# Kernel optimization log

Measured on AMD Instinct MI355X. Metric: run time of the kernel, lower is better.

## Reference

```python
import jax, jax.numpy as jnp
import numpy as np

K = 5  # kNN neighbors (includes self, as in PyG knn(x, x, k))


def _lin_bn(x, W, b, s, h):
    # Linear -> ReLU -> BatchNorm (inference, folded to scale s / shift h)
    return jax.nn.relu(x @ W + b) * s + h


def _knn_idx(x, k):
    # x: [B, N, F] -> idx: [B, N, k] indices of k nearest points (incl. self)
    x2 = jnp.sum(x * x, axis=-1)  # [B, N]
    d = x2[:, :, None] + x2[:, None, :] - 2.0 * jnp.einsum('bnf,bmf->bnm', x, x)
    return jax.lax.top_k(-d, k)[1]


def _edge_conv(x, k, edge_mlp):
    # DynamicEdgeConv: knn graph, message mlp([x_i, x_j - x_i]), max-aggregate
    idx = _knn_idx(x, k)                                   # [B, N, k]
    xj = jax.vmap(lambda xb, ib: xb[ib])(x, idx)           # [B, N, k, F]
    xi = jnp.broadcast_to(x[:, :, None, :], xj.shape)
    e = jnp.concatenate([xi, xj - xi], axis=-1)            # [B, N, k, 2F]
    return jnp.max(edge_mlp(e), axis=2)                    # [B, N, F_out]


def _forward(pos, w1a, b1a, s1a, h1a, w1b, b1b, s1b, h1b, w1c, b1c, s1c, h1c,
             w2, b2, s2, h2, wl, bl, sl, hl,
             wm1, bm1, sm1, hm1, wm2, bm2, sm2, hm2, wout, bout):
    mlp1 = lambda e: _lin_bn(_lin_bn(_lin_bn(e, w1a, b1a, s1a, h1a),
                                     w1b, b1b, s1b, h1b), w1c, b1c, s1c, h1c)
    mlp2 = lambda e: _lin_bn(e, w2, b2, s2, h2)
    x1 = _edge_conv(pos, K, mlp1)                          # [B, N, 64]
    x2 = _edge_conv(x1, K, mlp2)                           # [B, N, 128]
    out = _lin_bn(jnp.concatenate([x1, x2], axis=-1), wl, bl, sl, hl)  # [B,N,1024]
    out = jnp.max(out, axis=1)                             # global max pool -> [B,1024]
    out = _lin_bn(out, wm1, bm1, sm1, hm1)                 # Dropout = identity (eval)
    out = _lin_bn(out, wm2, bm2, sm2, hm2)
    return out @ wout + bout                               # [B, n_classes]


def setup_inputs() -> dict:
    key = jax.random.key(0)
    ks = jax.random.split(key, 32)
    B, N = 32, 2048
    rn = lambda k, sh: jax.random.normal(k, sh, dtype=jnp.float32)
    ru = lambda k, sh: jax.random.uniform(k, sh, dtype=jnp.float32)
    d = {'pos': rn(ks[0], (B, N, 3))}
    i = 1
    for nm, cin, cout in [('1a', 6, 64), ('1b', 64, 64), ('1c', 64, 64),
                          ('2', 128, 128), ('l', 192, 1024),
                          ('m1', 1024, 512), ('m2', 512, 256)]:
        d['w' + nm] = rn(ks[i], (cin, cout)) / np.sqrt(cin); i += 1
        d['b' + nm] = rn(ks[i], (cout,)) * 0.1; i += 1
        d['s' + nm] = ru(ks[i], (cout,)) + 0.5; i += 1
        d['h' + nm] = rn(ks[i], (cout,)) * 0.1; i += 1
    d['wout'] = rn(ks[i], (256, 2)) / np.sqrt(256.0); i += 1
    d['bout'] = rn(ks[i], (2,)) * 0.1
    return d


def reference(pos, w1a, b1a, s1a, h1a, w1b, b1b, s1b, h1b, w1c, b1c, s1c, h1c,
              w2, b2, s2, h2, wl, bl, sl, hl,
              wm1, bm1, sm1, hm1, wm2, bm2, sm2, hm2, wout, bout):
    return _forward(pos, w1a, b1a, s1a, h1a, w1b, b1b, s1b, h1b, w1c, b1c, s1c, h1c,
                    w2, b2, s2, h2, wl, bl, sl, hl,
                    wm1, bm1, sm1, hm1, wm2, bm2, sm2, hm2, wout, bout)
```

## Files before the change

kernel.cpp:

```cpp
#include <hip/hip_runtime.h>

#define DEV __device__ __forceinline__
DEV float relu_(float x) { return fmaxf(x, 0.0f); }

typedef __attribute__((ext_vector_type(4))) float f32x4;
typedef __attribute__((ext_vector_type(8))) __bf16 bf16x8;

DEV unsigned short bfbits(__bf16 b) { union { unsigned short s; __bf16 b; } x; x.b = b; return x.s; }
DEV __bf16 bffrom(unsigned short s) { union { unsigned short s; __bf16 b; } x; x.s = s; return x.b; }

DEV void knn_insert(float (&bd)[5], int (&bi)[5], float d, int j) {
  if (d >= bd[4]) return;
  bd[4] = d; bi[4] = j;
#pragma unroll
  for (int p = 4; p > 0; --p) {
    if (bd[p] < bd[p - 1]) {
      float td = bd[p]; bd[p] = bd[p - 1]; bd[p - 1] = td;
      int ti = bi[p]; bi[p] = bi[p - 1]; bi[p - 1] = ti;
    }
  }
}

DEV void knn_insert_bl(float (&bd)[5], int (&bi)[5], float d, int j) {
#pragma unroll
  for (int p = 0; p < 5; ++p) {
    bool lt = d < bd[p];
    float nd = lt ? d : bd[p];
    float cd = lt ? bd[p] : d;
    int ni = lt ? j : bi[p];
    int ci = lt ? bi[p] : j;
    bd[p] = nd; d = cd;
    bi[p] = ni; j = ci;
  }
}

DEV void ins5(float (&b)[5], float x) {
  b[4] = __builtin_amdgcn_fmed3f(b[3], b[4], x);
  b[3] = __builtin_amdgcn_fmed3f(b[2], b[3], x);
  b[2] = __builtin_amdgcn_fmed3f(b[1], b[2], x);
  b[1] = __builtin_amdgcn_fmed3f(b[0], b[1], x);
  b[0] = fminf(b[0], x);
}

__global__ __launch_bounds__(256) void k_front(
    const float* __restrict__ pos, const float* __restrict__ w1a,
    const float* __restrict__ b1a, const float* __restrict__ w1b,
    const float* __restrict__ w1c, const float* __restrict__ w2,
    const float* __restrict__ wl,
    int* __restrict__ idx1, float* __restrict__ uR, float* __restrict__ vR,
    __bf16* __restrict__ wfh, __bf16* __restrict__ wfl,
    __bf16* __restrict__ wph, __bf16* __restrict__ wpl,
    __bf16* __restrict__ wlb) {
  __shared__ __align__(16) float smem[9472];
  int tid = threadIdx.x;
  int blk = blockIdx.x;
  if (blk < 2048) {
    float* ps = smem;
    float* sqs = smem + 6144;
    float* md = smem + 8192;
    int* mi = (int*)(smem + 8832);
    int b = blk >> 6, qc = blk & 63;
    const float* src = pos + b * 6144;
    for (int u = tid; u < 6144; u += 256) ps[u] = src[u];
    __syncthreads();
    for (int u = tid; u < 2048; u += 256) {
      float x = ps[u * 3], y = ps[u * 3 + 1], z = ps[u * 3 + 2];
      sqs[u] = fmaf(z, z, fmaf(y, y, x * x));
    }
    __syncthreads();
    int q = tid & 31, sub = tid >> 5;
    int qi = qc * 32 + q;
    float qx = ps[qi * 3], qy = ps[qi * 3 + 1], qz = ps[qi * 3 + 2];
    float qsq = sqs[qi];
    float bp[5] = {1e30f, 1e30f, 1e30f, 1e30f, 1e30f};
    int j0 = sub * 256;
    for (int j = j0; j < j0 + 256; ++j) {
      float px = ps[j * 3], py = ps[j * 3 + 1], pz = ps[j * 3 + 2];
      float dot = fmaf(qz, pz, fmaf(qy, py, qx * px));
      float d = fmaxf((qsq + sqs[j]) - 2.0f * dot, 0.0f);
      unsigned u = (__float_as_uint(d) & 0xFFFFFF00u) | (unsigned)(j & 255);
      ins5(bp, __uint_as_float(u));
    }
    float bd[5]; int bi[5];
#pragma unroll
    for (int k = 0; k < 5; ++k) {
      unsigned u = __float_as_uint(bp[k]);
      bd[k] = __uint_as_float(u & 0xFFFFFF00u);
      bi[k] = j0 + (int)(u & 255u);
    }
    for (int half = 4; half >= 1; half >>= 1) {
      __syncthreads();
      if (sub >= half && sub < 2 * half) {
        int slot = (q * 4 + (sub - half)) * 5;
#pragma unroll
        for (int k = 0; k < 5; ++k) { md[slot + k] = bd[k]; mi[slot + k] = bi[k]; }
      }
      __syncthreads();
      if (sub < half) {
        int slot = (q * 4 + sub) * 5;
#pragma unroll
        for (int k = 0; k < 5; ++k) knn_insert_bl(bd, bi, md[slot + k], mi[slot + k]);
      }
    }
    if (sub == 0) {
      int* op = idx1 + (b * 2048 + qi) * 5;
#pragma unroll
      for (int k = 0; k < 5; ++k) op[k] = bi[k];
    }
  } else if (blk < 3072) {
    float* wAs = smem;
    float* bs = smem + 384;
    float* uS = smem + 448;
    float* vS = smem + 4800;
    for (int u = tid; u < 384; u += 256) wAs[u] = w1a[u];
    if (tid < 64) bs[tid] = b1a[tid];
    __syncthreads();
    int lane = tid & 63, fq = tid >> 6;
    int p0 = (blk - 2048) * 64;
    int p = p0 + lane;
    float x0 = pos[p * 3], x1 = pos[p * 3 + 1], x2 = pos[p * 3 + 2];
#pragma unroll
    for (int m = 0; m < 16; ++m) {
      int f = fq * 16 + m;
      float wt0 = wAs[f], wt1 = wAs[64 + f], wt2 = wAs[128 + f];
      float wb0 = wAs[192 + f], wb1 = wAs[256 + f], wb2 = wAs[320 + f];
      float uval = bs[f];
      uval = fmaf(x0, wt0 - wb0, uval);
      uval = fmaf(x1, wt1 - wb1, uval);
      uval = fmaf(x2, wt2 - wb2, uval);
      uS[lane * 68 + f] = uval;
      vS[lane * 68 + f] = fmaf(x2, wb2, fmaf(x1, wb1, x0 * wb0));
    }
    __syncthreads();
#pragma unroll
    for (int it = 0; it < 4; ++it) {
      int g = it * 1024 + tid * 4;
      int pl = g >> 6, f = g & 63;
      float4 uu = *(const float4*)(uS + pl * 68 + f);
      float4 vv = *(const float4*)(vS + pl * 68 + f);
      *(float4*)(uR + (size_t)p0 * 64 + g) = uu;
      *(float4*)(vR + (size_t)p0 * 64 + g) = vv;
    }
  } else {
    int pblk = blk - 3072;
    if (pblk < 4) {
      int t = pblk * 256 + tid;
      int m = t >> 9;
      int rem = t & 511;
      int nb = rem >> 7;
      int rem2 = rem & 127;
      int s = rem2 >> 6, lane = rem2 & 63;
      int k0 = s * 32 + (lane >> 4) * 8;
      int c = nb * 16 + (lane & 15);
      const float* W = m ? w1c : w1b;
      __bf16 oh[8], ol[8];
#pragma unroll
      for (int j = 0; j < 8; ++j) {
        float val = W[(k0 + j) * 64 + c];
        __bf16 h = (__bf16)val;
        oh[j] = h;
        ol[j] = (__bf16)(val - (float)h);
      }
      size_t off = (size_t)m * 4096 + ((size_t)((nb * 2 + s) * 64 + lane)) * 8;
      *(uint4*)(wfh + off) = *(const uint4*)oh;
      *(uint4*)(wfl + off) = *(const uint4*)ol;
    } else if (pblk < 12) {
      int t = (pblk - 4) * 256 + tid;
      int nb = t >> 7;
      int rem = t & 127;
      int ks = rem >> 6, lane = rem & 63;
      int k0 = ks * 32 + (lane >> 4) * 8;
      int col16 = lane & 15;
      __bf16 oh[8], ol[8];
#pragma unroll
      for (int j = 0; j < 8; ++j) {
        int k = k0 + j;
        float val;
        if (nb < 8) {
          int c = nb * 16 + col16;
          val = w2[k * 128 + c] - w2[(64 + k) * 128 + c];
        } else {
          int c = (nb - 8) * 16 + col16;
          val = w2[(64 + k) * 128 + c];
        }
        __bf16 h = (__bf16)val;
        oh[j] = h;
        ol[j] = (__bf16)(val - (float)h);
      }
      *(uint4*)(wph + (size_t)t * 8) = *(const uint4*)oh;
      *(uint4*)(wpl + (size_t)t * 8) = *(const uint4*)ol;
    } else {
      int t = (pblk - 12) * 256 + tid;
      int nt = t / 3072;
      int rem = t - nt * 3072;
      int ks = rem / 512;
      int rem2 = rem - ks * 512;
      int nb = rem2 >> 6, lane = rem2 & 63;
      int k0 = ks * 32 + (lane >> 4) * 8;
      int n = nt * 128 + nb * 16 + (lane & 15);
      __bf16 o[8];
#pragma unroll
      for (int j = 0; j < 8; ++j) o[j] = (__bf16)wl[(k0 + j) * 1024 + n];
      *(uint4*)(wlb + (size_t)t * 8) = *(const uint4*)o;
    }
  }
}

__global__ __launch_bounds__(256) void k_edge1(
    const int* __restrict__ idx1, const float* __restrict__ uR,
    const float* __restrict__ vR,
    const float* __restrict__ s1a, const float* __restrict__ h1a,
    const float* __restrict__ b1b, const float* __restrict__ s1b,
    const float* __restrict__ h1b,
    const float* __restrict__ b1c, const float* __restrict__ s1c,
    const float* __restrict__ h1c,
    const __bf16* __restrict__ wfh, const __bf16* __restrict__ wfl,
    __bf16* __restrict__ xh, __bf16* __restrict__ xl,
    float* __restrict__ sqo, __bf16* __restrict__ xb) {
  __shared__ __align__(16) __bf16 Wh[8192], Wl[8192];
  __shared__ __align__(16) unsigned h2b[4 * 1088];
  int tid = threadIdx.x;
  int w = tid >> 6, lane = tid & 63;
  int quad = lane >> 4, lm = lane & 15;
#pragma unroll
  for (int it = 0; it < 4; ++it) {
    int u4 = it * 256 + tid;
    *(uint4*)(Wh + (size_t)u4 * 8) = *(const uint4*)(wfh + (size_t)u4 * 8);
    *(uint4*)(Wl + (size_t)u4 * 8) = *(const uint4*)(wfl + (size_t)u4 * 8);
  }
  int p0 = blockIdx.x * 64;
  int b = p0 >> 11;
  size_t bb = (size_t)b * 2048;
  int edge = p0 + w * 16 + lm;
  float sA[2][8], hA[2][8];
#pragma unroll
  for (int s = 0; s < 2; ++s)
#pragma unroll
    for (int j = 0; j < 8; ++j) {
      int k = s * 32 + quad * 8 + j;
      sA[s][j] = s1a[k]; hA[s][j] = h1a[k];
    }
  float bB[4], sB[4], hB[4], bC[4], sC[4], hC[4];
#pragma unroll
  for (int nb = 0; nb < 4; ++nb) {
    int c = nb * 16 + lm;
    bB[nb] = b1b[c]; sB[nb] = s1b[c]; hB[nb] = h1b[c];
    bC[nb] = b1c[c]; sC[nb] = s1c[c]; hC[nb] = h1c[c];
  }
  unsigned* h2w = h2b + w * 1088;
  f32x4 mmax[4];
#pragma unroll
  for (int nb = 0; nb < 4; ++nb)
    mmax[nb] = (f32x4){-3.4e38f, -3.4e38f, -3.4e38f, -3.4e38f};
  __syncthreads();
  const float* urow = uR + (size_t)edge * 64;
  for (int kk = 0; kk < 5; ++kk) {
    int jn = idx1[edge * 5 + kk];
    const float* vrow = vR + (bb + jn) * 64;
    bf16x8 Ah[2], Al[2];
#pragma unroll
    for (int s = 0; s < 2; ++s) {
      int off = s * 32 + quad * 8;
      float4 u0 = *(const float4*)(urow + off);
      float4 u1 = *(const float4*)(urow + off + 4);
      float4 v0 = *(const float4*)(vrow + off);
      float4 v1 = *(const float4*)(vrow + off + 4);
      float uv[8] = {u0.x + v0.x, u0.y + v0.y, u0.z + v0.z, u0.w + v0.w,
                     u1.x + v1.x, u1.y + v1.y, u1.z + v1.z, u1.w + v1.w};
      __bf16 th[8], tl[8];
#pragma unroll
      for (int j = 0; j < 8; ++j) {
        float val = relu_(uv[j]) * sA[s][j] + hA[s][j];
        __bf16 hb = (__bf16)val;
        th[j] = hb;
        tl[j] = (__bf16)(val - (float)hb);
      }
      Ah[s] = *(const bf16x8*)th;
      Al[s] = *(const bf16x8*)tl;
    }
#pragma unroll
    for (int nb = 0; nb < 4; ++nb) {
      bf16x8 Bh0 = *(const bf16x8*)(Wh + ((size_t)((nb * 2 + 0) * 64 + lane)) * 8);
      bf16x8 Bh1 = *(const bf16x8*)(Wh + ((size_t)((nb * 2 + 1) * 64 + lane)) * 8);
      bf16x8 Bl0 = *(const bf16x8*)(Wl + ((size_t)((nb * 2 + 0) * 64 + lane)) * 8);
      bf16x8 Bl1 = *(const bf16x8*)(Wl + ((size_t)((nb * 2 + 1) * 64 + lane)) * 8);
      f32x4 a2 = {0.f, 0.f, 0.f, 0.f};
      a2 = __builtin_amdgcn_mfma_f32_16x16x32_bf16(Ah[0], Bh0, a2, 0, 0, 0);
      a2 = __builtin_amdgcn_mfma_f32_16x16x32_bf16(Ah[1], Bh1, a2, 0, 0, 0);
      a2 = __builtin_amdgcn_mfma_f32_16x16x32_bf16(Ah[0], Bl0, a2, 0, 0, 0);
      a2 = __builtin_amdgcn_mfma_f32_16x16x32_bf16(Ah[1], Bl1, a2, 0, 0, 0);
      a2 = __builtin_amdgcn_mfma_f32_16x16x32_bf16(Al[0], Bh0, a2, 0, 0, 0);
      a2 = __builtin_amdgcn_mfma_f32_16x16x32_bf16(Al[1], Bh1, a2, 0, 0, 0);
#pragma unroll
      for (int r = 0; r < 4; ++r) {
        float vv2 = relu_(a2[r] + bB[nb]) * sB[nb] + hB[nb];
        __bf16 hb = (__bf16)vv2;
        __bf16 lb = (__bf16)(vv2 - (float)hb);
        h2w[(quad * 4 + r) * 68 + nb * 16 + lm] =
            (unsigned)bfbits(hb) | ((unsigned)bfbits(lb) << 16);
      }
    }
    bf16x8 A3h[2], A3l[2];
#pragma unroll
    for (int s = 0; s < 2; ++s) {
      const unsigned* rp = h2w + lm * 68 + s * 32 + quad * 8;
      uint4 da = *(const uint4*)rp;
      uint4 db = *(const uint4*)(rp + 4);
      unsigned dw[8] = {da.x, da.y, da.z, da.w, db.x, db.y, db.z, db.w};
      __bf16 th[8], tl[8];
#pragma unroll
      for (int j = 0; j < 8; ++j) {
        th[j] = bffrom((unsigned short)(dw[j] & 0xFFFFu));
        tl[j] = bffrom((unsigned short)(dw[j] >> 16));
      }
      A3h[s] = *(const bf16x8*)th;
      A3l[s] = *(const bf16x8*)tl;
    }
#pragma unroll
    for (int nb = 0; nb < 4; ++nb) {
      bf16x8 Bh0 = *(const bf16x8*)(Wh + 4096 + ((size_t)((nb * 2 + 0) * 64 + lane)) * 8);
      bf16x8 Bh1 = *(const bf16x8*)(Wh + 4096 + ((size_t)((nb * 2 + 1) * 64 + lane)) * 8);
      bf16x8 Bl0 = *(const bf16x8*)(Wl + 4096 + ((size_t)((nb * 2 + 0) * 64 + lane)) * 8);
      bf16x8 Bl1 = *(const bf16x8*)(Wl + 4096 + ((size_t)((nb * 2 + 1) * 64 + lane)) * 8);
      f32x4 a3 = {0.f, 0.f, 0.f, 0.f};
      a3 = __builtin_amdgcn_mfma_f32_16x16x32_bf16(A3h[0], Bh0, a3, 0, 0, 0);
      a3 = __builtin_amdgcn_mfma_f32_16x16x32_bf16(A3h[1], Bh1, a3, 0, 0, 0);
      a3 = __builtin_amdgcn_mfma_f32_16x16x32_bf16(A3h[0], Bl0, a3, 0, 0, 0);
      a3 = __builtin_amdgcn_mfma_f32_16x16x32_bf16(A3h[1], Bl1, a3, 0, 0, 0);
      a3 = __builtin_amdgcn_mfma_f32_16x16x32_bf16(A3l[0], Bh0, a3, 0, 0, 0);
      a3 = __builtin_amdgcn_mfma_f32_16x16x32_bf16(A3l[1], Bh1, a3, 0, 0, 0);
#pragma unroll
      for (int r = 0; r < 4; ++r) mmax[nb][r] = fmaxf(mmax[nb][r], a3[r]);
    }
  }
  float sqp[4] = {0.f, 0.f, 0.f, 0.f};
#pragma unroll
  for (int nb = 0; nb < 4; ++nb) {
    int c = nb * 16 + lm;
#pragma unroll
    for (int r = 0; r < 4; ++r) {
      float vv3 = relu_(mmax[nb][r] + bC[nb]) * sC[nb] + hC[nb];
      sqp[r] = fmaf(vv3, vv3, sqp[r]);
      __bf16 hb = (__bf16)vv3;
      __bf16 lb = (__bf16)(vv3 - (float)hb);
      int n = p0 + w * 16 + quad * 4 + r;
      xh[(size_t)n * 64 + c] = hb;
      xl[(size_t)n * 64 + c] = lb;
      xb[(size_t)n * 192 + c] = hb;
    }
  }
#pragma unroll
  for (int r = 0; r < 4; ++r) {
    float s = sqp[r];
    s += __shfl_xor(s, 1);
    s += __shfl_xor(s, 2);
    s += __shfl_xor(s, 4);
    s += __shfl_xor(s, 8);
    if (lm == 0) sqo[p0 + w * 16 + quad * 4 + r] = s;
  }
}

__global__ __launch_bounds__(256) void k_mid(const __bf16* __restrict__ xh,
                                             const __bf16* __restrict__ xl,
                                             const float* __restrict__ sq,
                                             __bf16* __restrict__ scratch,
                                             const __bf16* __restrict__ wph,
                                             const __bf16* __restrict__ wpl,
                                             __bf16* __restrict__ Pb,
                                             __bf16* __restrict__ Qb) {
  __shared__ __align__(16) float smem[6656];
  int tid = threadIdx.x;
  int w = tid >> 6, lane = tid & 63;
  int quad = lane >> 4, lm = lane & 15;
  if (blockIdx.x < 2048) {
    __bf16* Bh = (__bf16*)smem;
    __bf16* Bl = (__bf16*)(smem + 2304);
    float* sqs = smem + 4608;
    int blk = blockIdx.x;
    int b = blk >> 6;
    int w6 = blk & 63;
    int qc = w6 >> 1, g = w6 & 1;
    int q0 = qc * 64;
    size_t bb = (size_t)b * 2048;
    for (int u = tid; u < 512; u += 256)
      *(float4*)(sqs + u * 4) = *(const float4*)(sq + bb + u * 4);
    const __bf16* qh = xh + (bb + q0 + w * 16 + lm) * 64 + quad * 8;
    const __bf16* ql = xl + (bb + q0 + w * 16 + lm) * 64 + quad * 8;
    bf16x8 Ah0 = *(const bf16x8*)(qh);
    bf16x8 Ah1 = *(const bf16x8*)(qh + 32);
    bf16x8 Al0 = *(const bf16x8*)(ql);
    bf16x8 Al1 = *(const bf16x8*)(ql + 32);
    __syncthreads();
    float qsq[4];
#pragma unroll
    for (int r = 0; r < 4; ++r) qsq[r] = sqs[q0 + w * 16 + quad * 4 + r];
    float bp[4][5];
#pragma unroll
    for (int r = 0; r < 4; ++r)
#pragma unroll
      for (int k = 0; k < 5; ++k) bp[r][k] = 1e30f;
    for (int it = 0; it < 16; ++it) {
      int ct = g * 16 + it;
#pragma unroll
      for (int pass = 0; pass < 2; ++pass) {
        int unit = pass * 256 + tid;
        int n = unit >> 3, cc = unit & 7;
        const __bf16* gsrc = xh + (bb + ct * 64 + n) * 64 + cc * 8;
        const __bf16* gsrl = xl + (bb + ct * 64 + n) * 64 + cc * 8;
        *(uint4*)(Bh + n * 72 + cc * 8) = *(const uint4*)gsrc;
        *(uint4*)(Bl + n * 72 + cc * 8) = *(const uint4*)gsrl;
      }
      __syncthreads();
#pragma unroll
      for (int nt = 0; nt < 4; ++nt) {
        const __bf16* bph = Bh + (nt * 16 + lm) * 72 + quad * 8;
        const __bf16* bpl = Bl + (nt * 16 + lm) * 72 + quad * 8;
        bf16x8 Bh0 = *(const bf16x8*)(bph);
        bf16x8 Bh1 = *(const bf16x8*)(bph + 32);
        bf16x8 Bl0 = *(const bf16x8*)(bpl);
        bf16x8 Bl1 = *(const bf16x8*)(bpl + 32);
        f32x4 acc = {0.f, 0.f, 0.f, 0.f};
        acc = __builtin_amdgcn_mfma_f32_16x16x32_bf16(Ah0, Bh0, acc, 0, 0, 0);
        acc = __builtin_amdgcn_mfma_f32_16x16x32_bf16(Ah1, Bh1, acc, 0, 0, 0);
        acc = __builtin_amdgcn_mfma_f32_16x16x32_bf16(Ah0, Bl0, acc, 0, 0, 0);
        acc = __builtin_amdgcn_mfma_f32_16x16x32_bf16(Ah1, Bl1, acc, 0, 0, 0);
        acc = __builtin_amdgcn_mfma_f32_16x16x32_bf16(Al0, Bh0, acc, 0, 0, 0);
        acc = __builtin_amdgcn_mfma_f32_16x16x32_bf16(Al1, Bh1, acc, 0, 0, 0);
        float csq = sqs[ct * 64 + nt * 16 + lm];
        unsigned key = (unsigned)(it * 4 + nt);
#pragma unroll
        for (int r = 0; r < 4; ++r) {
          float d = fmaxf((qsq[r] + csq) - 2.0f * acc[r], 0.0f);
          unsigned u = (__float_as_uint(d) & 0xFFFFFFC0u) | key;
          ins5(bp[r], __uint_as_float(u));
        }
      }
      __syncthreads();
    }
    float bd[4][5];
    int bi[4][5];
#pragma unroll
    for (int r = 0; r < 4; ++r)
#pragma unroll
      for (int k = 0; k < 5; ++k) {
        unsigned u = __float_as_uint(bp[r][k]);
        bd[r][k] = __uint_as_float(u & 0xFFFFFFC0u);
        bi[r][k] = (g << 10) + (((int)(u & 63u)) << 4) + lm;
      }
    for (int m = 1; m <= 8; m <<= 1) {
#pragma unroll
      for (int r = 0; r < 4; ++r) {
        float od[5]; int oi[5];
#pragma unroll
        for (int k = 0; k < 5; ++k) {
          od[k] = __shfl_xor(bd[r][k], m);
          oi[k] = __shfl_xor(bi[r][k], m);
        }
#pragma unroll
        for (int k = 0; k < 5; ++k) knn_insert(bd[r], bi[r], od[k], oi[k]);
      }
    }
    if (lm == 0) {
#pragma unroll
      for (int r = 0; r < 4; ++r) {
        int qi = q0 + w * 16 + quad * 4 + r;
        uint2* sp = (uint2*)((char*)scratch + (size_t)(bb + qi) * 384 + 128 + g * 40);
#pragma unroll
        for (int k = 0; k < 5; ++k) {
          uint2 v;
          v.x = __float_as_uint(bd[r][k]);
          v.y = (unsigned)bi[r][k];
          sp[k] = v;
        }
      }
    }
  } else {
    __bf16* Wh = (__bf16*)smem;
    __bf16* Wl = (__bf16*)(smem + 2048);
    int n0 = (blockIdx.x - 2048) * 64;
    const __bf16* ah = xh + (size_t)(n0 + w * 16 + lm) * 64 + quad * 8;
    const __bf16* al = xl + (size_t)(n0 + w * 16 + lm) * 64 + quad * 8;
    bf16x8 Ah0 = *(const bf16x8*)(ah);
    bf16x8 Ah1 = *(const bf16x8*)(ah + 32);
    bf16x8 Al0 = *(const bf16x8*)(al);
    bf16x8 Al1 = *(const bf16x8*)(al + 32);
    for (int chunk = 0; chunk < 4; ++chunk) {
      __syncthreads();
#pragma unroll
      for (int it = 0; it < 2; ++it) {
        int unit = it * 256 + tid;
        *(uint4*)(Wh + (size_t)unit * 8) =
            *(const uint4*)(wph + (size_t)chunk * 4096 + (size_t)unit * 8);
        *(uint4*)(Wl + (size_t)unit * 8) =
            *(const uint4*)(wpl + (size_t)chunk * 4096 + (size_t)unit * 8);
      }
      __syncthreads();
#pragma unroll
      for (int nb4 = 0; nb4 < 4; ++nb4) {
        int nb = chunk * 4 + nb4;
        bf16x8 Bh0 = *(const bf16x8*)(Wh + ((size_t)(nb4 * 2 + 0) * 64 + lane) * 8);
        bf16x8 Bh1 = *(const bf16x8*)(Wh + ((size_t)(nb4 * 2 + 1) * 64 + lane) * 8);
        bf16x8 Bl0 = *(const bf16x8*)(Wl + ((size_t)(nb4 * 2 + 0) * 64 + lane) * 8);
        bf16x8 Bl1 = *(const bf16x8*)(Wl + ((size_t)(nb4 * 2 + 1) * 64 + lane) * 8);
        f32x4 acc = {0.f, 0.f, 0.f, 0.f};
        acc = __builtin_amdgcn_mfma_f32_16x16x32_bf16(Ah0, Bh0, acc, 0, 0, 0);
        acc = __builtin_amdgcn_mfma_f32_16x16x32_bf16(Ah1, Bh1, acc, 0, 0, 0);
        acc = __builtin_amdgcn_mfma_f32_16x16x32_bf16(Ah0, Bl0, acc, 0, 0, 0);
        acc = __builtin_amdgcn_mfma_f32_16x16x32_bf16(Ah1, Bl1, acc, 0, 0, 0);
        acc = __builtin_amdgcn_mfma_f32_16x16x32_bf16(Al0, Bh0, acc, 0, 0, 0);
        acc = __builtin_amdgcn_mfma_f32_16x16x32_bf16(Al1, Bh1, acc, 0, 0, 0);
        bool isP = (nb < 8);
        __bf16* base = isP ? Pb : Qb;
        int col = (isP ? nb : nb - 8) * 16 + lm;
#pragma unroll
        for (int r = 0; r < 4; ++r) {
          int n = n0 + w * 16 + quad * 4 + r;
          base[(size_t)n * 128 + col] = (__bf16)acc[r];
        }
      }
    }
  }
}

__global__ __launch_bounds__(256) void k_kmerge(const __bf16* __restrict__ scratch,
                                                int* __restrict__ idx2) {
  int n = blockIdx.x * 256 + threadIdx.x;
  const uint2* sp = (const uint2*)((const char*)scratch + (size_t)n * 384 + 128);
  float bd[5]; int bi[5];
#pragma unroll
  for (int k = 0; k < 5; ++k) {
    uint2 v = sp[k];
    bd[k] = __uint_as_float(v.x);
    bi[k] = (int)v.y;
  }
#pragma unroll
  for (int k = 0; k < 5; ++k) {
    uint2 v = sp[5 + k];
    knn_insert(bd, bi, __uint_as_float(v.x), (int)v.y);
  }
  int* op = idx2 + (size_t)n * 5;
#pragma unroll
  for (int k = 0; k < 5; ++k) op[k] = bi[k];
}

__global__ __launch_bounds__(256) void k_gmax(const __bf16* __restrict__ Pb,
                                              const __bf16* __restrict__ Qb,
                                              const int* __restrict__ idx2,
                                              const float* __restrict__ b2,
                                              const float* __restrict__ s2,
                                              const float* __restrict__ h2v,
                                              __bf16* __restrict__ xb) {
  int tid = threadIdx.x;
  int c4 = tid & 31, p = tid >> 5;
  int n = blockIdx.x * 8 + p;
  int b = n >> 11;
  const int* ip = idx2 + n * 5;
  int c0 = c4 * 4;
  float m[4] = {-3.4e38f, -3.4e38f, -3.4e38f, -3.4e38f};
#pragma unroll
  for (int k = 0; k < 5; ++k) {
    int j = ip[k];
    uint2 q = *(const uint2*)(Qb + ((size_t)(b * 2048 + j)) * 128 + c0);
    m[0] = fmaxf(m[0], (float)bffrom((unsigned short)(q.x & 0xFFFFu)));
    m[1] = fmaxf(m[1], (float)bffrom((unsigned short)(q.x >> 16)));
    m[2] = fmaxf(m[2], (float)bffrom((unsigned short)(q.y & 0xFFFFu)));
    m[3] = fmaxf(m[3], (float)bffrom((unsigned short)(q.y >> 16)));
  }
  uint2 pv = *(const uint2*)(Pb + (size_t)n * 128 + c0);
  float pvf[4] = {(float)bffrom((unsigned short)(pv.x & 0xFFFFu)),
                  (float)bffrom((unsigned short)(pv.x >> 16)),
                  (float)bffrom((unsigned short)(pv.y & 0xFFFFu)),
                  (float)bffrom((unsigned short)(pv.y >> 16))};
  __bf16 o[4];
#pragma unroll
  for (int i = 0; i < 4; ++i) {
    float v = pvf[i] + m[i] + b2[c0 + i];
    o[i] = (__bf16)(relu_(v) * s2[c0 + i] + h2v[c0 + i]);
  }
  uint2 ov;
  ov.x = (unsigned)bfbits(o[0]) | ((unsigned)bfbits(o[1]) << 16);
  ov.y = (unsigned)bfbits(o[2]) | ((unsigned)bfbits(o[3]) << 16);
  *(uint2*)(xb + (size_t)n * 192 + 64 + c0) = ov;
}

__global__ __launch_bounds__(256) void k_linl_mfma(const __bf16* __restrict__ xb,
                                                   const __bf16* __restrict__ wlb,
                                                   float* __restrict__ pool_part) {
  __shared__ __align__(16) __bf16 Aall[12288];
  __shared__ __align__(16) __bf16 Bl[8192];
  int tid = threadIdx.x;
  int w = tid >> 6, lane = tid & 63;
  int mg = blockIdx.x;
  int n0 = mg << 6;
  int quad = lane >> 4, lm = lane & 15;
#pragma unroll
  for (int it = 0; it < 6; ++it) {
    int unit = it * 256 + tid;
    int mb = unit / 384;
    int rem = unit - mb * 384;
    int ks = rem >> 6, ln = rem & 63;
    int lmm = ln & 15, qd = ln >> 4;
    const uint4* ga = (const uint4*)(xb + (size_t)(n0 + mb * 16 + lmm) * 192 + ks * 32 + qd * 8);
    *(uint4*)(Aall + ((size_t)(mb * 6 + ks) * 64 + ln) * 8) = *ga;
  }
  for (int ng = 0; ng < 4; ++ng) {
    f32x4 acc[4][4];
#pragma unroll
    for (int i = 0; i < 4; ++i)
#pragma unroll
      for (int j = 0; j < 4; ++j) acc[i][j] = (f32x4){0.f, 0.f, 0.f, 0.f};
    for (int ks = 0; ks < 6; ++ks) {
      __syncthreads();
#pragma unroll
      for (int nt2 = 0; nt2 < 2; ++nt2) {
#pragma unroll
        for (int u = 0; u < 2; ++u) {
          int unit = u * 256 + tid;
          const uint4* gb = (const uint4*)(wlb + ((size_t)((ng * 2 + nt2) * 6 + ks)) * 4096 + (size_t)unit * 8);
          *(uint4*)(Bl + (size_t)nt2 * 4096 + (size_t)unit * 8) = *gb;
        }
      }
      __syncthreads();
      bf16x8 af[4], bfr[4];
#pragma unroll
      for (int i = 0; i < 4; ++i)
        af[i] = *(const bf16x8*)(Aall + ((size_t)(i * 6 + ks) * 64 + lane) * 8);
      int nt2 = w >> 1, nbb = (w & 1) * 4;
#pragma unroll
      for (int j = 0; j < 4; ++j)
        bfr[j] = *(const bf16x8*)(Bl + (size_t)nt2 * 4096 + ((size_t)((nbb + j) * 64 + lane)) * 8);
#pragma unroll
      for (int i = 0; i < 4; ++i)
#pragma unroll
        for (int j = 0; j < 4; ++j)
          acc[i][j] = __builtin_amdgcn_mfma_f32_16x16x32_bf16(af[i], bfr[j], acc[i][j], 0, 0, 0);
    }
#pragma unroll
    for (int j = 0; j < 4; ++j) {
      float m = -3.4e38f;
#pragma unroll
      for (int i = 0; i < 4; ++i)
#pragma unroll
        for (int r = 0; r < 4; ++r) m = fmaxf(m, acc[i][j][r]);
      m = fmaxf(m, __shfl_xor(m, 16));
      m = fmaxf(m, __shfl_xor(m, 32));
      if (quad == 0) {
        int ch = ng * 256 + (w >> 1) * 128 + (w & 1) * 64 + j * 16 + lm;
        pool_part[(size_t)mg * 1024 + ch] = m;
      }
    }
  }
}

__global__ __launch_bounds__(256) void k_pool(const float* __restrict__ pool_part,
                                              const float* __restrict__ bl,
                                              const float* __restrict__ sl,
                                              const float* __restrict__ hl,
                                              float* __restrict__ p,
                                              float* __restrict__ out) {
  int b = blockIdx.x >> 2, cb = blockIdx.x & 3;
  int c = cb * 256 + threadIdx.x;
  const float* src = pool_part + (size_t)(b * 32) * 1024 + c;
  float m0 = -3.4e38f, m1 = -3.4e38f, m2 = -3.4e38f, m3 = -3.4e38f;
#pragma unroll
  for (int t = 0; t < 32; t += 4) {
    m0 = fmaxf(m0, src[(size_t)t * 1024]);
    m1 = fmaxf(m1, src[(size_t)(t + 1) * 1024]);
    m2 = fmaxf(m2, src[(size_t)(t + 2) * 1024]);
    m3 = fmaxf(m3, src[(size_t)(t + 3) * 1024]);
  }
  float m = fmaxf(fmaxf(m0, m1), fmaxf(m2, m3));
  p[b * 1024 + c] = relu_(m + bl[c]) * sl[c] + hl[c];
  if (blockIdx.x == 0 && threadIdx.x < 64) out[threadIdx.x] = 0.0f;
}

__global__ __launch_bounds__(256) void k_m1(const float* __restrict__ p,
                                            const float* __restrict__ wm1,
                                            const float* __restrict__ bm1,
                                            const float* __restrict__ sm1,
                                            const float* __restrict__ hm1,
                                            float* __restrict__ h1) {
  __shared__ float p_s[1024];
  __shared__ float red[4][64];
  int b = blockIdx.x >> 3, cb = blockIdx.x & 7;
  int tid = threadIdx.x;
  for (int u = tid; u < 1024; u += 256) p_s[u] = p[b * 1024 + u];
  __syncthreads();
  int c64 = tid & 63, q = tid >> 6;
  int C = cb * 64 + c64;
  int f0 = q * 256;
  const float* W = wm1 + (size_t)f0 * 512 + C;
  float a[8] = {0.f, 0.f, 0.f, 0.f, 0.f, 0.f, 0.f, 0.f};
  for (int f = 0; f < 256; f += 8) {
#pragma unroll
    for (int u = 0; u < 8; ++u)
      a[u] = fmaf(p_s[f0 + f + u], W[(size_t)(f + u) * 512], a[u]);
  }
  red[q][c64] = ((a[0] + a[1]) + (a[2] + a[3])) + ((a[4] + a[5]) + (a[6] + a[7]));
  __syncthreads();
  if (tid < 64) {
    float t = (red[0][tid] + red[1][tid]) + (red[2][tid] + red[3][tid]);
    int C2 = cb * 64 + tid;
    h1[b * 512 + C2] = relu_(t + bm1[C2]) * sm1[C2] + hm1[C2];
  }
}

__global__ __launch_bounds__(256) void k_m2o(const float* __restrict__ h1,
                                             const float* __restrict__ wm2,
                                             const float* __restrict__ bm2,
                                             const float* __restrict__ sm2,
                                             const float* __restrict__ hm2,
                                             const float* __restrict__ wout,
                                             const float* __restrict__ bout,
                                             float* __restrict__ out) {
  __shared__ float h1_s[512];
  __shared__ float red[4][64];
  int b = blockIdx.x >> 2, cb = blockIdx.x & 3;
  int tid = threadIdx.x;
  for (int u = tid; u < 512; u += 256) h1_s[u] = h1[b * 512 + u];
  __syncthreads();
  int c64 = tid & 63, q = tid >> 6;
  int C = cb * 64 + c64;
  int f0 = q * 128;
  const float* W = wm2 + (size_t)f0 * 256 + C;
  float a[4] = {0.f, 0.f, 0.f, 0.f};
  for (int f = 0; f < 128; f += 4) {
#pragma unroll
    for (int u = 0; u < 4; ++u)
      a[u] = fmaf(h1_s[f0 + f + u], W[(size_t)(f + u) * 256], a[u]);
  }
  red[q][c64] = (a[0] + a[1]) + (a[2] + a[3]);
  __syncthreads();
  if (tid < 64) {
    float t = (red[0][tid] + red[1][tid]) + (red[2][tid] + red[3][tid]);
    int C2 = cb * 64 + tid;
    float h2v = relu_(t + bm2[C2]) * sm2[C2] + hm2[C2];
    float2 wv = *(const float2*)(wout + C2 * 2);
    float v0 = h2v * wv.x, v1 = h2v * wv.y;
#pragma unroll
    for (int m = 1; m < 64; m <<= 1) {
      v0 += __shfl_xor(v0, m);
      v1 += __shfl_xor(v1, m);
    }
    if (tid == 0) {
      if (cb == 0) { v0 += bout[0]; v1 += bout[1]; }
      atomicAdd(&out[b * 2], v0);
      atomicAdd(&out[b * 2 + 1], v1);
    }
  }
}

extern "C" void kernel_launch(void* const* d_in, const int* in_sizes, int n_in,
                              void* d_out, int out_size, void* d_ws, size_t ws_size,
                              hipStream_t stream) {
  const float* pos = (const float*)d_in[0];
  const float* w1a = (const float*)d_in[1];
  const float* b1a = (const float*)d_in[2];
  const float* s1a = (const float*)d_in[3];
  const float* h1a = (const float*)d_in[4];
  const float* w1b = (const float*)d_in[5];
  const float* b1b = (const float*)d_in[6];
  const float* s1b = (const float*)d_in[7];
  const float* h1b = (const float*)d_in[8];
  const float* w1c = (const float*)d_in[9];
  const float* b1c = (const float*)d_in[10];
  const float* s1c = (const float*)d_in[11];
  const float* h1c = (const float*)d_in[12];
  const float* w2 = (const float*)d_in[13];
  const float* b2 = (const float*)d_in[14];
  const float* s2 = (const float*)d_in[15];
  const float* h2 = (const float*)d_in[16];
  const float* wl = (const float*)d_in[17];
  const float* bl = (const float*)d_in[18];
  const float* sl = (const float*)d_in[19];
  const float* hl = (const float*)d_in[20];
  const float* wm1 = (const float*)d_in[21];
  const float* bm1 = (const float*)d_in[22];
  const float* sm1 = (const float*)d_in[23];
  const float* hm1 = (const float*)d_in[24];
  const float* wm2 = (const float*)d_in[25];
  const float* bm2 = (const float*)d_in[26];
  const float* sm2 = (const float*)d_in[27];
  const float* hm2 = (const float*)d_in[28];
  const float* wout = (const float*)d_in[29];
  const float* bout = (const float*)d_in[30];
  float* out = (float*)d_out;

  float* base = (float*)d_ws;
  __bf16* xh = (__bf16*)base;
  __bf16* xl = (__bf16*)(base + 2097152);
  float* PbF = base + 4194304;
  float* QbF = PbF + 4194304;
  float* xbF = QbF + 4194304;
  int* idx = (int*)(xbF + 6291456);
  float* sq = (float*)(idx + 327680);
  __bf16* wph = (__bf16*)(sq + 65536);
  __bf16* wpl = (__bf16*)(sq + 65536 + 8192);
  __bf16* wfh = (__bf16*)(sq + 65536 + 16384);
  __bf16* wfl = (__bf16*)(sq + 65536 + 20480);
  __bf16* wlb = (__bf16*)(sq + 65536 + 24576);
  __bf16* Pb = (__bf16*)PbF;
  __bf16* Qb = (__bf16*)QbF;
  __bf16* xb = (__bf16*)xbF;
  float* uR = PbF;
  float* vR = QbF;
  float* pool_part = base + 131072;
  float* p_pool = base + 1179648;
  float* h1g = base + 1212416;

  k_front<<<3180, 256, 0, stream>>>(pos, w1a, b1a, w1b, w1c, w2, wl, idx, uR, vR,
                                    wfh, wfl, wph, wpl, wlb);
  k_edge1<<<1024, 256, 0, stream>>>(idx, uR, vR, s1a, h1a, b1b, s1b, h1b, b1c,
                                    s1c, h1c, wfh, wfl, xh, xl, sq, xb);
  k_mid<<<3072, 256, 0, stream>>>(xh, xl, sq, xb, wph, wpl, Pb, Qb);
  k_kmerge<<<256, 256, 0, stream>>>(xb, idx);
  k_gmax<<<8192, 256, 0, stream>>>(Pb, Qb, idx, b2, s2, h2, xb);
  k_linl_mfma<<<1024, 256, 0, stream>>>(xb, wlb, pool_part);
  k_pool<<<128, 256, 0, stream>>>(pool_part, bl, sl, hl, p_pool, out);
  k_m1<<<256, 256, 0, stream>>>(p_pool, wm1, bm1, sm1, hm1, h1g);
  k_m2o<<<128, 256, 0, stream>>>(h1g, wm2, bm2, sm2, hm2, wout, bout, out);
}
```

Before: 363.2 us.

## Transpose point cloud to SoA, prefetch kNN tiles, merge top-5 with sorting network

```diff
diff --git a/kernel.cpp b/kernel.cpp
--- a/kernel.cpp
+++ b/kernel.cpp
@@ -40,6 +40,18 @@
   b[2] = __builtin_amdgcn_fmed3f(b[1], b[2], x);
   b[1] = __builtin_amdgcn_fmed3f(b[0], b[1], x);
   b[0] = fminf(b[0], x);
+}
+
+DEV void merge_net5(float (&a)[5], float b0, float b1, float b2, float b3, float b4) {
+  float c0 = fminf(a[0], b0);
+  float c1 = fminf(fminf(b1, a[1]), fmaxf(a[0], b0));
+  float c2 = fminf(fminf(b2, a[2]), fminf(fmaxf(a[0], b1), fmaxf(a[1], b0)));
+  float c3 = fminf(fminf(b3, a[3]),
+                   fminf(fmaxf(a[0], b2), fminf(fmaxf(a[1], b1), fmaxf(a[2], b0))));
+  float c4 = fminf(fminf(b4, a[4]),
+                   fminf(fminf(fmaxf(a[0], b3), fmaxf(a[1], b2)),
+                         fminf(fmaxf(a[2], b1), fmaxf(a[3], b0))));
+  a[0] = c0; a[1] = c1; a[2] = c2; a[3] = c3; a[4] = c4;
 }
 
 __global__ __launch_bounds__(256) void k_front(
@@ -55,31 +67,46 @@
   int tid = threadIdx.x;
   int blk = blockIdx.x;
   if (blk < 2048) {
-    float* ps = smem;
+    float* xs = smem;
     float* sqs = smem + 6144;
     float* md = smem + 8192;
     int* mi = (int*)(smem + 8832);
     int b = blk >> 6, qc = blk & 63;
     const float* src = pos + b * 6144;
-    for (int u = tid; u < 6144; u += 256) ps[u] = src[u];
+    for (int u = tid; u < 6144; u += 256) {
+      float v = src[u];
+      int p = u / 3, c = u - p * 3;
+      smem[c * 2048 + p] = v;
+    }
     __syncthreads();
     for (int u = tid; u < 2048; u += 256) {
-      float x = ps[u * 3], y = ps[u * 3 + 1], z = ps[u * 3 + 2];
+      float x = xs[u], y = xs[2048 + u], z = xs[4096 + u];
       sqs[u] = fmaf(z, z, fmaf(y, y, x * x));
     }
     __syncthreads();
     int q = tid & 31, sub = tid >> 5;
     int qi = qc * 32 + q;
-    float qx = ps[qi * 3], qy = ps[qi * 3 + 1], qz = ps[qi * 3 + 2];
+    float qx = xs[qi], qy = xs[2048 + qi], qz = xs[4096 + qi];
     float qsq = sqs[qi];
     float bp[5] = {1e30f, 1e30f, 1e30f, 1e30f, 1e30f};
     int j0 = sub * 256;
-    for (int j = j0; j < j0 + 256; ++j) {
-      float px = ps[j * 3], py = ps[j * 3 + 1], pz = ps[j * 3 + 2];
-      float dot = fmaf(qz, pz, fmaf(qy, py, qx * px));
-      float d = fmaxf((qsq + sqs[j]) - 2.0f * dot, 0.0f);
-      unsigned u = (__float_as_uint(d) & 0xFFFFFF00u) | (unsigned)(j & 255);
-      ins5(bp, __uint_as_float(u));
+    for (int j4 = 0; j4 < 64; ++j4) {
+      int jb = j0 + j4 * 4;
+      float4 xv = *(const float4*)(xs + jb);
+      float4 yv = *(const float4*)(xs + 2048 + jb);
+      float4 zv = *(const float4*)(xs + 4096 + jb);
+      float4 sv = *(const float4*)(sqs + jb);
+      float xa[4] = {xv.x, xv.y, xv.z, xv.w};
+      float ya[4] = {yv.x, yv.y, yv.z, yv.w};
+      float za[4] = {zv.x, zv.y, zv.z, zv.w};
+      float sa[4] = {sv.x, sv.y, sv.z, sv.w};
+#pragma unroll
+      for (int c = 0; c < 4; ++c) {
+        float dot = fmaf(qz, za[c], fmaf(qy, ya[c], qx * xa[c]));
+        float d = fmaxf((qsq + sa[c]) - 2.0f * dot, 0.0f);
+        unsigned u = (__float_as_uint(d) & 0xFFFFFF00u) | (unsigned)(j4 * 4 + c);
+        ins5(bp, __uint_as_float(u));
+      }
     }
     float bd[5]; int bi[5];
 #pragma unroll
@@ -390,6 +417,17 @@
     bf16x8 Ah1 = *(const bf16x8*)(qh + 32);
     bf16x8 Al0 = *(const bf16x8*)(ql);
     bf16x8 Al1 = *(const bf16x8*)(ql + 32);
+    int nu = tid >> 3, cu = tid & 7;
+    const __bf16* ph0 = xh + (bb + (size_t)g * 1024 + nu) * 64 + cu * 8;
+    const __bf16* pl0 = xl + (bb + (size_t)g * 1024 + nu) * 64 + cu * 8;
+    __bf16* dh0 = Bh + nu * 72 + cu * 8;
+    __bf16* dh1 = Bh + (nu + 32) * 72 + cu * 8;
+    __bf16* dl0 = Bl + nu * 72 + cu * 8;
+    __bf16* dl1 = Bl + (nu + 32) * 72 + cu * 8;
+    uint4 rh0 = *(const uint4*)(ph0);
+    uint4 rh1 = *(const uint4*)(ph0 + 2048);
+    uint4 rl0 = *(const uint4*)(pl0);
+    uint4 rl1 = *(const uint4*)(pl0 + 2048);
     __syncthreads();
     float qsq[4];
 #pragma unroll
@@ -400,17 +438,20 @@
 #pragma unroll
       for (int k = 0; k < 5; ++k) bp[r][k] = 1e30f;
     for (int it = 0; it < 16; ++it) {
+      *(uint4*)dh0 = rh0;
+      *(uint4*)dh1 = rh1;
+      *(uint4*)dl0 = rl0;
+      *(uint4*)dl1 = rl1;
+      __syncthreads();
+      if (it < 15) {
+        const __bf16* p1 = ph0 + (it + 1) * 4096;
+        const __bf16* p2 = pl0 + (it + 1) * 4096;
+        rh0 = *(const uint4*)(p1);
+        rh1 = *(const uint4*)(p1 + 2048);
+        rl0 = *(const uint4*)(p2);
+        rl1 = *(const uint4*)(p2 + 2048);
+      }
       int ct = g * 16 + it;
-#pragma unroll
-      for (int pass = 0; pass < 2; ++pass) {
-        int unit = pass * 256 + tid;
-        int n = unit >> 3, cc = unit & 7;
-        const __bf16* gsrc = xh + (bb + ct * 64 + n) * 64 + cc * 8;
-        const __bf16* gsrl = xl + (bb + ct * 64 + n) * 64 + cc * 8;
-        *(uint4*)(Bh + n * 72 + cc * 8) = *(const uint4*)gsrc;
-        *(uint4*)(Bl + n * 72 + cc * 8) = *(const uint4*)gsrl;
-      }
-      __syncthreads();
 #pragma unroll
       for (int nt = 0; nt < 4; ++nt) {
         const __bf16* bph = Bh + (nt * 16 + lm) * 72 + quad * 8;
@@ -437,6 +478,27 @@
       }
       __syncthreads();
     }
+#pragma unroll
+    for (int r = 0; r < 4; ++r)
+#pragma unroll
+      for (int k = 0; k < 5; ++k) {
+        unsigned u = __float_as_uint(bp[r][k]);
+        bp[r][k] = __uint_as_float((u & 0xFFFFFF00u) | ((u & 63u) << 2) |
+                                   (unsigned)(lm & 3));
+      }
+#pragma unroll
+    for (int m = 1; m <= 2; m <<= 1) {
+#pragma unroll
+      for (int r = 0; r < 4; ++r) {
+        float b0 = __shfl_xor(bp[r][0], m);
+        float b1 = __shfl_xor(bp[r][1], m);
+        float b2 = __shfl_xor(bp[r][2], m);
+        float b3 = __shfl_xor(bp[r][3], m);
+        float b4 = __shfl_xor(bp[r][4], m);
+        merge_net5(bp[r], b0, b1, b2, b3, b4);
+      }
+    }
+    int lmb = lm & ~3;
     float bd[4][5];
     int bi[4][5];
 #pragma unroll
@@ -444,10 +506,12 @@
 #pragma unroll
       for (int k = 0; k < 5; ++k) {
         unsigned u = __float_as_uint(bp[r][k]);
-        bd[r][k] = __uint_as_float(u & 0xFFFFFFC0u);
-        bi[r][k] = (g << 10) + (((int)(u & 63u)) << 4) + lm;
-      }
-    for (int m = 1; m <= 8; m <<= 1) {
+        bd[r][k] = __uint_as_float(u & 0xFFFFFF00u);
+        unsigned k8 = u & 255u;
+        bi[r][k] = (g << 10) | (((int)(k8 >> 2)) << 4) | (lmb | (int)(k8 & 3));
+      }
+#pragma unroll
+    for (int m = 4; m <= 8; m <<= 1) {
 #pragma unroll
       for (int r = 0; r < 4; ++r) {
         float od[5]; int oi[5];
```

New measurement: 356.9 us (median of 2 runs). About the same (-1.7%).
